# Performance work log

Hardware: AMD Instinct MI355X
Metric: run time of the kernel (lower is better)

The kernel has to match this reference:

```python
import jax, jax.numpy as jnp
import numpy as np

N = 50000
E = 800000
D = 128


def setup_inputs() -> dict:
    key = jax.random.key(0)
    ks = jax.random.split(key, 10)
    x = jax.random.normal(ks[0], (N, D), dtype=jnp.float32)
    edge_index = jax.random.randint(ks[1], (2, E), 0, N, dtype=jnp.int32)
    s = 1.0 / np.sqrt(D)
    W1 = jax.random.uniform(ks[2], (D, D), jnp.float32, -s, s)
    b1 = jnp.zeros((D,), jnp.float32)
    W2 = jax.random.uniform(ks[3], (D, D), jnp.float32, -s, s)
    b2 = jnp.zeros((D,), jnp.float32)
    Wt = jax.random.uniform(ks[4], (D, 1), jnp.float32, -s, s)
    bt = jnp.zeros((1,), jnp.float32)
    We = jax.random.uniform(ks[5], (D, 1), jnp.float32, -s, s)
    be = jnp.zeros((1,), jnp.float32)
    return {"x": x, "edge_index": edge_index, "W1": W1, "b1": b1,
            "W2": W2, "b2": b2, "Wt": Wt, "bt": bt, "We": We, "be": be}


def _gcn_norm(edge_index, n):
    # add self-loops, then symmetric normalization D^-1/2 (A+I) D^-1/2
    loop = jnp.arange(n, dtype=edge_index.dtype)
    src = jnp.concatenate([edge_index[0], loop])
    dst = jnp.concatenate([edge_index[1], loop])
    ones = jnp.ones(src.shape[0], dtype=jnp.float32)
    deg = jax.ops.segment_sum(ones, dst, num_segments=n)
    dinv = jnp.where(deg > 0, jax.lax.rsqrt(deg), 0.0)
    norm = dinv[src] * dinv[dst]  # [E+N]
    return src, dst, norm


def _gcn_conv(h, W, b, src, dst, norm, n):
    h = h @ W                                   # [N, D'] dense GEMM
    msg = h[src] * norm[:, None]                # gather + scale
    out = jax.ops.segment_sum(msg, dst, num_segments=n)  # scatter-add
    return out + b


def reference(x, edge_index, W1, b1, W2, b2, Wt, bt, We, be):
    n = x.shape[0]
    src, dst, norm = _gcn_norm(edge_index, n)
    h = jax.nn.relu(_gcn_conv(x, W1, b1, src, dst, norm, n))
    h = jax.nn.relu(_gcn_conv(h, W2, b2, src, dst, norm, n))
    # dropout is identity at inference (eval mode)
    survival_time = h @ Wt + bt   # [N, 1]
    event_status = h @ We + be    # [N, 1]
    return survival_time, event_status
```

## Files before the change

### kernel.cpp

```cpp
#include <hip/hip_runtime.h>
#include <hip/hip_fp16.h>
#include <math.h>

#define NN 50000
#define NE 800000
#define DD 128

#define NB  196
#define CAP 5300
#define EPB 4096
#define A_BLOCKS 196

#define SLAB2 (NN * 64)

typedef _Float16 half8_t __attribute__((ext_vector_type(8)));
typedef float f32x4 __attribute__((ext_vector_type(4)));


__global__ __launch_bounds__(256) void k_setup(const int* __restrict__ src, const int* __restrict__ dst,
                                               int* __restrict__ bcnt, unsigned int* __restrict__ ebuf,
                                               const float* __restrict__ W1, const float* __restrict__ W2,
                                               __half* __restrict__ WT1, __half* __restrict__ WT2) {
    const int blk = blockIdx.x;
    const int tid = threadIdx.x;

    if (blk < A_BLOCKS) {
        __shared__ int hist[256];
        __shared__ int scanbuf[256];
        __shared__ int gbase[256];
        __shared__ unsigned int stage[EPB];
        __shared__ int tgt[EPB];

        const int e0 = blk * EPB;
        int nE = NE - e0; if (nE > EPB) nE = EPB;

        hist[tid] = 0;
        __syncthreads();

        unsigned int pk[16];
        unsigned int br[16];
        #pragma unroll
        for (int j = 0; j < 16; ++j) {
            int idx = tid + j * 256;
            if (idx < nE) {
                int e = e0 + idx;
                int s = src[e], d = dst[e];
                int b = d >> 8;
                int r = atomicAdd(&hist[b], 1);
                pk[j] = (unsigned int)s | ((unsigned int)(d & 255) << 16);
                br[j] = (unsigned int)b | ((unsigned int)r << 8);
            }
        }
        __syncthreads();
        int v = hist[tid];
        scanbuf[tid] = v;
        __syncthreads();
        for (int o = 1; o < 256; o <<= 1) {
            int t2 = (tid >= o) ? scanbuf[tid - o] : 0;
            __syncthreads();
            scanbuf[tid] += t2;
            __syncthreads();
        }
        int base_excl = scanbuf[tid] - v;
        if (tid < NB && v > 0) gbase[tid] = tid * CAP + atomicAdd(&bcnt[tid], v);
        hist[tid] = base_excl;
        __syncthreads();

        #pragma unroll
        for (int j = 0; j < 16; ++j) {
            int idx = tid + j * 256;
            if (idx < nE) {
                int b = br[j] & 255;
                int r = (int)(br[j] >> 8);
                int pos = hist[b] + r;
                stage[pos] = pk[j];
                tgt[pos]   = gbase[b] + r;
            }
        }
        __syncthreads();
        #pragma unroll
        for (int j = 0; j < 16; ++j) {
            int idx = tid + j * 256;
            if (idx < nE) ebuf[tgt[idx]] = stage[idx];
        }
    } else {
        const float* W  = (blk == A_BLOCKS) ? W1 : W2;
        __half*      WT = (blk == A_BLOCKS) ? WT1 : WT2;
        int n = tid >> 1;
        int k0 = (tid & 1) * 64;
        #pragma unroll 8
        for (int j = 0; j < 64; ++j) {
            int k = k0 + j;
            WT[n * DD + k] = __float2half(W[k * DD + n]);
        }
    }
}


__global__ __launch_bounds__(512) void k_build_csr(const unsigned int* __restrict__ ebuf,
                                                   const int* __restrict__ bcnt,
                                                   int* __restrict__ row_ptr,
                                                   float* __restrict__ dinv,
                                                   unsigned short* __restrict__ col) {
    __shared__ int cnt[256];
    __shared__ int scanb[256];
    __shared__ unsigned short stage[CAP];

    const int b   = blockIdx.x;
    const int tid = threadIdx.x;
    const int seg0 = b * CAP;
    const int sb   = bcnt[b];
    const int n0   = b << 8;
    int nb = NN - n0; if (nb > 256) nb = 256;

    if (tid < 256) scanb[tid] = (tid < NB) ? bcnt[tid] : 0;
    __syncthreads();
    for (int o = 1; o < 256; o <<= 1) {
        int t = 0;
        if (tid < 256 && tid >= o) t = scanb[tid - o];
        __syncthreads();
        if (tid < 256) scanb[tid] += t;
        __syncthreads();
    }
    const int rbase = scanb[b] - sb;
    __syncthreads();

    if (tid < 256) cnt[tid] = 0;
    __syncthreads();
    for (int p = tid; p < sb; p += 512) {
        unsigned int e = ebuf[seg0 + p];
        atomicAdd(&cnt[(e >> 16) & 255], 1);
    }
    __syncthreads();
    int v = (tid < 256) ? cnt[tid] : 0;
    if (tid < 256) scanb[tid] = v;
    __syncthreads();
    for (int o = 1; o < 256; o <<= 1) {
        int t = 0;
        if (tid < 256 && tid >= o) t = scanb[tid - o];
        __syncthreads();
        if (tid < 256) scanb[tid] += t;
        __syncthreads();
    }
    int excl = (tid < 256) ? (scanb[tid] - v) : 0;
    if (tid < nb) {
        row_ptr[n0 + tid] = rbase + excl;
        dinv[n0 + tid] = rsqrtf(1.0f + (float)v);
    }
    if (b == 0 && tid == 0) row_ptr[NN] = NE;
    if (tid < 256) cnt[tid] = excl;
    __syncthreads();
    for (int p = tid; p < sb; p += 512) {
        unsigned int e = ebuf[seg0 + p];
        int pos = atomicAdd(&cnt[(e >> 16) & 255], 1);
        stage[pos] = (unsigned short)(e & 0xFFFFu);
    }
    __syncthreads();
    for (int p = tid; p < sb; p += 512) {
        col[rbase + p] = stage[p];
    }
}


#define LPAD 136
#define GEMM_B 782
#define ZERO_B 98

__global__ __launch_bounds__(256) void k_gemm_x(const float* __restrict__ X, const __half* __restrict__ WT,
                                                const float* __restrict__ dinv, __half* __restrict__ Gc,
                                                float* __restrict__ zbuf, int zcount) {
    const int tid = threadIdx.x;

    if (blockIdx.x >= GEMM_B) {
        int idx = (blockIdx.x - GEMM_B) * 256 + tid;
        if (idx * 4 + 3 < zcount) ((float4*)zbuf)[idx] = make_float4(0.f, 0.f, 0.f, 0.f);
        else {
            for (int k = idx * 4; k < zcount; ++k) zbuf[k] = 0.f;
        }
        return;
    }

    __shared__ __half Wl[DD * LPAD];
    __shared__ __half Al[64 * LPAD];

    const int row0 = blockIdx.x * 64;

    {
        const uint4* WTg = (const uint4*)WT;
        #pragma unroll
        for (int j = 0; j < 8; ++j) {
            int u = tid + j * 256;
            int n = u >> 4, koff = (u & 15) * 8;
            uint4 v = WTg[u];
            *(uint4*)&Wl[n * LPAD + koff] = v;
        }
    }
    {
        const float4* X4 = (const float4*)X;
        #pragma unroll
        for (int j = 0; j < 8; ++j) {
            int u = tid + j * 256;
            int r = u >> 5, c4 = u & 31;
            int grow = row0 + r;
            float4 v = make_float4(0.f, 0.f, 0.f, 0.f);
            if (grow < NN) v = X4[(size_t)grow * 32 + c4];
            __half2 a = __floats2half2_rn(v.x, v.y);
            __half2 b = __floats2half2_rn(v.z, v.w);
            uint2 pk;
            pk.x = *(unsigned int*)&a;
            pk.y = *(unsigned int*)&b;
            *(uint2*)&Al[r * LPAD + c4 * 4] = pk;
        }
    }
    __syncthreads();

    const int wave = tid >> 6;
    const int lane = tid & 63;
    const int m    = lane & 15;
    const int quad = lane >> 4;

    f32x4 acc[8];
    #pragma unroll
    for (int t = 0; t < 8; ++t) acc[t] = (f32x4){0.f, 0.f, 0.f, 0.f};

    #pragma unroll
    for (int kk = 0; kk < DD; kk += 32) {
        half8_t a = *(const half8_t*)&Al[(wave * 16 + m) * LPAD + kk + quad * 8];
        #pragma unroll
        for (int t = 0; t < 8; ++t) {
            half8_t b = *(const half8_t*)&Wl[(t * 16 + m) * LPAD + kk + quad * 8];
            acc[t] = __builtin_amdgcn_mfma_f32_16x16x32_f16(a, b, acc[t], 0, 0, 0);
        }
    }

    __syncthreads();

    float4 dv = *(const float4*)&dinv[row0 + wave * 16 + quad * 4];

    #pragma unroll
    for (int t = 0; t < 8; ++t) {
        #pragma unroll
        for (int r = 0; r < 4; ++r) {
            int row_l = wave * 16 + quad * 4 + r;
            int c     = t * 16 + m;
            float val = acc[t][r] * ((const float*)&dv)[r];
            Al[row_l * LPAD + c] = __float2half(val);
        }
    }
    __syncthreads();

    {
        #pragma unroll
        for (int j = 0; j < 4; ++j) {
            int u = tid + j * 256;
            int r = u >> 4, c16 = u & 15;
            int ch = c16 >> 3, wi = c16 & 7;
            int grow = row0 + r;
            if (grow < NN) {
                uint4 v = *(const uint4*)&Al[r * LPAD + c16 * 8];
                *(uint4*)(Gc + (size_t)ch * SLAB2 + (size_t)grow * 64 + wi * 8) = v;
            }
        }
    }
}


__global__ __launch_bounds__(256) void k_gemm_h(const __half* __restrict__ Xc, const __half* __restrict__ WT,
                                                const float* __restrict__ dinv, __half* __restrict__ Gc) {
    __shared__ __half Wl[DD * LPAD];
    __shared__ __half Al[64 * LPAD];

    const int tid  = threadIdx.x;
    const int row0 = blockIdx.x * 64;

    {
        const uint4* WTg = (const uint4*)WT;
        #pragma unroll
        for (int j = 0; j < 8; ++j) {
            int u = tid + j * 256;
            int n = u >> 4, koff = (u & 15) * 8;
            uint4 v = WTg[u];
            *(uint4*)&Wl[n * LPAD + koff] = v;
        }
    }
    {
        #pragma unroll
        for (int j = 0; j < 4; ++j) {
            int u = tid + j * 256;
            int r = u >> 4, c16 = u & 15;
            int ch = c16 >> 3, wi = c16 & 7;
            int grow = row0 + r;
            uint4 v;
            if (grow < NN) v = *(const uint4*)(Xc + (size_t)ch * SLAB2 + (size_t)grow * 64 + wi * 8);
            else { v.x = 0; v.y = 0; v.z = 0; v.w = 0; }
            *(uint4*)&Al[r * LPAD + c16 * 8] = v;
        }
    }
    __syncthreads();

    const int wave = tid >> 6;
    const int lane = tid & 63;
    const int m    = lane & 15;
    const int quad = lane >> 4;

    f32x4 acc[8];
    #pragma unroll
    for (int t = 0; t < 8; ++t) acc[t] = (f32x4){0.f, 0.f, 0.f, 0.f};

    #pragma unroll
    for (int kk = 0; kk < DD; kk += 32) {
        half8_t a = *(const half8_t*)&Al[(wave * 16 + m) * LPAD + kk + quad * 8];
        #pragma unroll
        for (int t = 0; t < 8; ++t) {
            half8_t b = *(const half8_t*)&Wl[(t * 16 + m) * LPAD + kk + quad * 8];
            acc[t] = __builtin_amdgcn_mfma_f32_16x16x32_f16(a, b, acc[t], 0, 0, 0);
        }
    }

    __syncthreads();

    float4 dv = *(const float4*)&dinv[row0 + wave * 16 + quad * 4];

    #pragma unroll
    for (int t = 0; t < 8; ++t) {
        #pragma unroll
        for (int r = 0; r < 4; ++r) {
            int row_l = wave * 16 + quad * 4 + r;
            int c     = t * 16 + m;
            float val = acc[t][r] * ((const float*)&dv)[r];
            Al[row_l * LPAD + c] = __float2half(val);
        }
    }
    __syncthreads();

    {
        #pragma unroll
        for (int j = 0; j < 4; ++j) {
            int u = tid + j * 256;
            int r = u >> 4, c16 = u & 15;
            int ch = c16 >> 3, wi = c16 & 7;
            int grow = row0 + r;
            if (grow < NN) {
                uint4 v = *(const uint4*)&Al[r * LPAD + c16 * 8];
                *(uint4*)(Gc + (size_t)ch * SLAB2 + (size_t)grow * 64 + wi * 8) = v;
            }
        }
    }
}


__device__ inline float4 h4_to_f4(uint2 r) {
    __half2 a = *(__half2*)&r.x;
    __half2 b = *(__half2*)&r.y;
    float2 lo = __half22float2(a), hi = __half22float2(b);
    return make_float4(lo.x, lo.y, hi.x, hi.y);
}

__device__ inline uint2 f4_to_h4(float4 v) {
    __half2 a = __floats2half2_rn(v.x, v.y);
    __half2 b = __floats2half2_rn(v.z, v.w);
    uint2 r;
    r.x = *(unsigned int*)&a;
    r.y = *(unsigned int*)&b;
    return r;
}

__device__ inline float4 gather_grp64(const __half* __restrict__ slab, int node, int fl,
                                      const unsigned short* __restrict__ col, int beg, int end) {
    const __half* base = slab + fl * 4;
    float4 accA = h4_to_f4(*(const uint2*)(base + (size_t)node * 64));
    float4 accB = make_float4(0.f, 0.f, 0.f, 0.f);
    int p = beg;
    for (; p + 7 < end; p += 8) {
        int s0 = col[p],     s1 = col[p + 1], s2 = col[p + 2], s3 = col[p + 3];
        int s4 = col[p + 4], s5 = col[p + 5], s6 = col[p + 6], s7 = col[p + 7];
        float4 v0 = h4_to_f4(*(const uint2*)(base + (size_t)s0 * 64));
        float4 v1 = h4_to_f4(*(const uint2*)(base + (size_t)s1 * 64));
        float4 v2 = h4_to_f4(*(const uint2*)(base + (size_t)s2 * 64));
        float4 v3 = h4_to_f4(*(const uint2*)(base + (size_t)s3 * 64));
        float4 v4 = h4_to_f4(*(const uint2*)(base + (size_t)s4 * 64));
        float4 v5 = h4_to_f4(*(const uint2*)(base + (size_t)s5 * 64));
        float4 v6 = h4_to_f4(*(const uint2*)(base + (size_t)s6 * 64));
        float4 v7 = h4_to_f4(*(const uint2*)(base + (size_t)s7 * 64));
        accA.x += (v0.x + v1.x) + (v4.x + v5.x);
        accA.y += (v0.y + v1.y) + (v4.y + v5.y);
        accA.z += (v0.z + v1.z) + (v4.z + v5.z);
        accA.w += (v0.w + v1.w) + (v4.w + v5.w);
        accB.x += (v2.x + v3.x) + (v6.x + v7.x);
        accB.y += (v2.y + v3.y) + (v6.y + v7.y);
        accB.z += (v2.z + v3.z) + (v6.z + v7.z);
        accB.w += (v2.w + v3.w) + (v6.w + v7.w);
    }
    if (p + 3 < end) {
        int s0 = col[p], s1 = col[p + 1], s2 = col[p + 2], s3 = col[p + 3];
        float4 v0 = h4_to_f4(*(const uint2*)(base + (size_t)s0 * 64));
        float4 v1 = h4_to_f4(*(const uint2*)(base + (size_t)s1 * 64));
        float4 v2 = h4_to_f4(*(const uint2*)(base + (size_t)s2 * 64));
        float4 v3 = h4_to_f4(*(const uint2*)(base + (size_t)s3 * 64));
        accA.x += v0.x + v1.x; accA.y += v0.y + v1.y; accA.z += v0.z + v1.z; accA.w += v0.w + v1.w;
        accB.x += v2.x + v3.x; accB.y += v2.y + v3.y; accB.z += v2.z + v3.z; accB.w += v2.w + v3.w;
        p += 4;
    }
    for (; p < end; ++p) {
        int s0 = col[p];
        float4 v0 = h4_to_f4(*(const uint2*)(base + (size_t)s0 * 64));
        accA.x += v0.x; accA.y += v0.y; accA.z += v0.z; accA.w += v0.w;
    }
    accA.x += accB.x; accA.y += accB.y; accA.z += accB.z; accA.w += accB.w;
    return accA;
}

__global__ __launch_bounds__(256) void k_aggregate_c(const __half* __restrict__ G, const float* __restrict__ dinv,
                                                     const int* __restrict__ row_ptr, const unsigned short* __restrict__ col,
                                                     const float* __restrict__ bias, __half* __restrict__ H) {
    const int bx    = blockIdx.x;
    const int slot  = bx & 7;
    const int chunk = slot >> 2;
    const int nb    = (bx >> 3) * 4 + (slot & 3);
    const int g     = threadIdx.x >> 4;
    const int fl    = threadIdx.x & 15;
    const int node  = nb * 16 + g;
    if (node >= NN) return;

    const __half* slab = G + (size_t)chunk * SLAB2;
    int beg = row_ptr[node];
    int end = row_ptr[node + 1];
    float4 acc = gather_grp64(slab, node, fl, col, beg, end);

    float di = dinv[node];
    float4 bv = *(const float4*)(bias + chunk * 64 + fl * 4);
    float4 hv;
    hv.x = fmaxf(fmaf(di, acc.x, bv.x), 0.f);
    hv.y = fmaxf(fmaf(di, acc.y, bv.y), 0.f);
    hv.z = fmaxf(fmaf(di, acc.z, bv.z), 0.f);
    hv.w = fmaxf(fmaf(di, acc.w, bv.w), 0.f);
    *(uint2*)(H + (size_t)chunk * SLAB2 + (size_t)node * 64 + fl * 4) = f4_to_h4(hv);
}

__global__ __launch_bounds__(256) void k_aggregate_heads_c(const __half* __restrict__ G, const float* __restrict__ dinv,
                                                           const int* __restrict__ row_ptr, const unsigned short* __restrict__ col,
                                                           const float* __restrict__ bias,
                                                           const float* __restrict__ Wt, const float* __restrict__ bt,
                                                           const float* __restrict__ We, const float* __restrict__ be,
                                                           float* __restrict__ out) {
    const int bx    = blockIdx.x;
    const int slot  = bx & 7;
    const int chunk = slot >> 2;
    const int nb    = (bx >> 3) * 4 + (slot & 3);
    const int g     = threadIdx.x >> 4;
    const int fl    = threadIdx.x & 15;
    const int node  = nb * 16 + g;
    if (node >= NN) return;

    const __half* slab = G + (size_t)chunk * SLAB2;
    int beg = row_ptr[node];
    int end = row_ptr[node + 1];
    float4 acc = gather_grp64(slab, node, fl, col, beg, end);

    float di = dinv[node];
    float4 bv = *(const float4*)(bias + chunk * 64 + fl * 4);
    float hx = fmaxf(fmaf(di, acc.x, bv.x), 0.f);
    float hy = fmaxf(fmaf(di, acc.y, bv.y), 0.f);
    float hz = fmaxf(fmaf(di, acc.z, bv.z), 0.f);
    float hw = fmaxf(fmaf(di, acc.w, bv.w), 0.f);

    float4 wt = *(const float4*)(Wt + chunk * 64 + fl * 4);
    float4 we = *(const float4*)(We + chunk * 64 + fl * 4);
    float t  = hx * wt.x + hy * wt.y + hz * wt.z + hw * wt.w;
    float ev = hx * we.x + hy * we.y + hz * we.z + hw * we.w;
    #pragma unroll
    for (int o = 1; o < 16; o <<= 1) {
        t  += __shfl_xor(t, o, 64);
        ev += __shfl_xor(ev, o, 64);
    }
    if (fl == 0) {
        if (chunk == 0) { t += bt[0]; ev += be[0]; }
        atomicAdd(&out[node], t);
        atomicAdd(&out[NN + node], ev);
    }
}


extern "C" void kernel_launch(void* const* d_in, const int* in_sizes, int n_in,
                              void* d_out, int out_size, void* d_ws, size_t ws_size,
                              hipStream_t stream) {
    const float* x  = (const float*)d_in[0];
    const int*   ei = (const int*)d_in[1];
    const float* W1 = (const float*)d_in[2];
    const float* b1 = (const float*)d_in[3];
    const float* W2 = (const float*)d_in[4];
    const float* b2 = (const float*)d_in[5];
    const float* Wt = (const float*)d_in[6];
    const float* bt = (const float*)d_in[7];
    const float* We = (const float*)d_in[8];
    const float* be = (const float*)d_in[9];
    float* out = (float*)d_out;

    const int* srcI = ei;
    const int* dstI = ei + NE;

    char* w = (char*)d_ws;
    __half*         Gh    = (__half*)w;         w += (size_t)NN * DD * sizeof(__half);
    __half*         H1h   = (__half*)w;         w += (size_t)NN * DD * sizeof(__half);
    __half*         WT1   = (__half*)w;         w += (size_t)DD * DD * sizeof(__half);
    __half*         WT2   = (__half*)w;         w += (size_t)DD * DD * sizeof(__half);
    unsigned int*   ebuf  = (unsigned int*)w;   w += (size_t)NB * CAP * sizeof(unsigned int);
    unsigned short* col   = (unsigned short*)w; w += (size_t)NE * sizeof(unsigned short);
    float*          dinv  = (float*)w;          w += (size_t)(NN + 64) * sizeof(float);
    int*            rowp  = (int*)w;            w += (size_t)(NN + 1) * sizeof(int);
    int*            bcnt  = (int*)w;            w += (size_t)NB * sizeof(int);

    const int SETUP_B = A_BLOCKS + 2;
    const int NBLK    = (NN + 15) / 16;
    const int AGG_B   = ((NBLK + 3) / 4) * 8;

    hipMemsetAsync(bcnt, 0, (size_t)NB * sizeof(int), stream);

    hipLaunchKernelGGL(k_setup,     dim3(SETUP_B), dim3(256), 0, stream,
                       srcI, dstI, bcnt, ebuf, W1, W2, WT1, WT2);
    hipLaunchKernelGGL(k_build_csr, dim3(NB),      dim3(512), 0, stream, ebuf, bcnt, rowp, dinv, col);

    hipLaunchKernelGGL(k_gemm_x,      dim3(GEMM_B + ZERO_B), dim3(256), 0, stream, x, WT1, dinv, Gh, out, out_size);
    hipLaunchKernelGGL(k_aggregate_c, dim3(AGG_B),           dim3(256), 0, stream, Gh, dinv, rowp, col, b1, H1h);

    hipLaunchKernelGGL(k_gemm_h,            dim3(GEMM_B), dim3(256), 0, stream, H1h, WT2, dinv, Gh);
    hipLaunchKernelGGL(k_aggregate_heads_c, dim3(AGG_B),  dim3(256), 0, stream, Gh, dinv, rowp, col, b2,
                       Wt, bt, We, be, out);
}
```

Measured before the change: 202.5 us.

## Pad CSR rows to multiples of eight with dummy node for vectorized gathers

Each CSR row is padded to a multiple of eight neighbors. Padding entries point to a dummy node NN, whose GEMM output row (padded slab NNP) is written unconditionally. This lets the aggregate loop load eight column indices as one uint4 and removes the tail loops and the global row-offset scan. The cost is extra gathers of padding rows and larger col storage, and correctness depends on the dummy row holding zeros, which the GEMM must write from padded input rows.

```diff
diff --git a/kernel.cpp b/kernel.cpp
--- a/kernel.cpp
+++ b/kernel.cpp
@@ -3,15 +3,17 @@
 #include <math.h>
 
 #define NN 50000
+#define NNP 50048
 #define NE 800000
 #define DD 128
 
 #define NB  196
 #define CAP 5300
+#define CAPP 6400
 #define EPB 4096
 #define A_BLOCKS 196
 
-#define SLAB2 (NN * 64)
+#define SLAB2 (NNP * 64)
 
 typedef _Float16 half8_t __attribute__((ext_vector_type(8)));
 typedef float f32x4 __attribute__((ext_vector_type(4)));
@@ -99,12 +101,12 @@
 
 __global__ __launch_bounds__(512) void k_build_csr(const unsigned int* __restrict__ ebuf,
                                                    const int* __restrict__ bcnt,
-                                                   int* __restrict__ row_ptr,
+                                                   int* __restrict__ rowbeg, int* __restrict__ rowend,
                                                    float* __restrict__ dinv,
                                                    unsigned short* __restrict__ col) {
     __shared__ int cnt[256];
     __shared__ int scanb[256];
-    __shared__ unsigned short stage[CAP];
+    __shared__ unsigned short stage[CAPP];
 
     const int b   = blockIdx.x;
     const int tid = threadIdx.x;
@@ -113,7 +115,16 @@
     const int n0   = b << 8;
     int nb = NN - n0; if (nb > 256) nb = 256;
 
-    if (tid < 256) scanb[tid] = (tid < NB) ? bcnt[tid] : 0;
+    if (tid < 256) cnt[tid] = 0;
+    __syncthreads();
+    for (int p = tid; p < sb; p += 512) {
+        unsigned int e = ebuf[seg0 + p];
+        atomicAdd(&cnt[(e >> 16) & 255], 1);
+    }
+    __syncthreads();
+    int v  = (tid < 256) ? cnt[tid] : 0;
+    int pv = (v + 7) & ~7;
+    if (tid < 256) scanb[tid] = pv;
     __syncthreads();
     for (int o = 1; o < 256; o <<= 1) {
         int t = 0;
@@ -122,33 +133,13 @@
         if (tid < 256) scanb[tid] += t;
         __syncthreads();
     }
-    const int rbase = scanb[b] - sb;
-    __syncthreads();
-
-    if (tid < 256) cnt[tid] = 0;
-    __syncthreads();
-    for (int p = tid; p < sb; p += 512) {
-        unsigned int e = ebuf[seg0 + p];
-        atomicAdd(&cnt[(e >> 16) & 255], 1);
-    }
-    __syncthreads();
-    int v = (tid < 256) ? cnt[tid] : 0;
-    if (tid < 256) scanb[tid] = v;
-    __syncthreads();
-    for (int o = 1; o < 256; o <<= 1) {
-        int t = 0;
-        if (tid < 256 && tid >= o) t = scanb[tid - o];
-        __syncthreads();
-        if (tid < 256) scanb[tid] += t;
-        __syncthreads();
-    }
-    int excl = (tid < 256) ? (scanb[tid] - v) : 0;
+    int exclp = (tid < 256) ? (scanb[tid] - pv) : 0;
     if (tid < nb) {
-        row_ptr[n0 + tid] = rbase + excl;
+        rowbeg[n0 + tid] = b * CAPP + exclp;
+        rowend[n0 + tid] = b * CAPP + exclp + pv;
         dinv[n0 + tid] = rsqrtf(1.0f + (float)v);
     }
-    if (b == 0 && tid == 0) row_ptr[NN] = NE;
-    if (tid < 256) cnt[tid] = excl;
+    if (tid < 256) cnt[tid] = exclp;
     __syncthreads();
     for (int p = tid; p < sb; p += 512) {
         unsigned int e = ebuf[seg0 + p];
@@ -156,8 +147,13 @@
         stage[pos] = (unsigned short)(e & 0xFFFFu);
     }
     __syncthreads();
-    for (int p = tid; p < sb; p += 512) {
-        col[rbase + p] = stage[p];
+    if (tid < nb) {
+        for (int k = exclp + v; k < exclp + pv; ++k) stage[k] = (unsigned short)NN;
+    }
+    __syncthreads();
+    const int sbp = scanb[255];
+    for (int p = tid; p < sbp; p += 512) {
+        col[b * CAPP + p] = stage[p];
     }
 }
 
@@ -256,10 +252,8 @@
             int r = u >> 4, c16 = u & 15;
             int ch = c16 >> 3, wi = c16 & 7;
             int grow = row0 + r;
-            if (grow < NN) {
-                uint4 v = *(const uint4*)&Al[r * LPAD + c16 * 8];
-                *(uint4*)(Gc + (size_t)ch * SLAB2 + (size_t)grow * 64 + wi * 8) = v;
-            }
+            uint4 v = *(const uint4*)&Al[r * LPAD + c16 * 8];
+            *(uint4*)(Gc + (size_t)ch * SLAB2 + (size_t)grow * 64 + wi * 8) = v;
         }
     }
 }
@@ -340,10 +334,8 @@
             int r = u >> 4, c16 = u & 15;
             int ch = c16 >> 3, wi = c16 & 7;
             int grow = row0 + r;
-            if (grow < NN) {
-                uint4 v = *(const uint4*)&Al[r * LPAD + c16 * 8];
-                *(uint4*)(Gc + (size_t)ch * SLAB2 + (size_t)grow * 64 + wi * 8) = v;
-            }
+            uint4 v = *(const uint4*)&Al[r * LPAD + c16 * 8];
+            *(uint4*)(Gc + (size_t)ch * SLAB2 + (size_t)grow * 64 + wi * 8) = v;
         }
     }
 }
@@ -370,10 +362,12 @@
     const __half* base = slab + fl * 4;
     float4 accA = h4_to_f4(*(const uint2*)(base + (size_t)node * 64));
     float4 accB = make_float4(0.f, 0.f, 0.f, 0.f);
-    int p = beg;
-    for (; p + 7 < end; p += 8) {
-        int s0 = col[p],     s1 = col[p + 1], s2 = col[p + 2], s3 = col[p + 3];
-        int s4 = col[p + 4], s5 = col[p + 5], s6 = col[p + 6], s7 = col[p + 7];
+    for (int p = beg; p < end; p += 8) {
+        uint4 c8 = *(const uint4*)(col + p);
+        int s0 = c8.x & 0xFFFF, s1 = c8.x >> 16;
+        int s2 = c8.y & 0xFFFF, s3 = c8.y >> 16;
+        int s4 = c8.z & 0xFFFF, s5 = c8.z >> 16;
+        int s6 = c8.w & 0xFFFF, s7 = c8.w >> 16;
         float4 v0 = h4_to_f4(*(const uint2*)(base + (size_t)s0 * 64));
         float4 v1 = h4_to_f4(*(const uint2*)(base + (size_t)s1 * 64));
         float4 v2 = h4_to_f4(*(const uint2*)(base + (size_t)s2 * 64));
@@ -391,27 +385,13 @@
         accB.z += (v2.z + v3.z) + (v6.z + v7.z);
         accB.w += (v2.w + v3.w) + (v6.w + v7.w);
     }
-    if (p + 3 < end) {
-        int s0 = col[p], s1 = col[p + 1], s2 = col[p + 2], s3 = col[p + 3];
-        float4 v0 = h4_to_f4(*(const uint2*)(base + (size_t)s0 * 64));
-        float4 v1 = h4_to_f4(*(const uint2*)(base + (size_t)s1 * 64));
-        float4 v2 = h4_to_f4(*(const uint2*)(base + (size_t)s2 * 64));
-        float4 v3 = h4_to_f4(*(const uint2*)(base + (size_t)s3 * 64));
-        accA.x += v0.x + v1.x; accA.y += v0.y + v1.y; accA.z += v0.z + v1.z; accA.w += v0.w + v1.w;
-        accB.x += v2.x + v3.x; accB.y += v2.y + v3.y; accB.z += v2.z + v3.z; accB.w += v2.w + v3.w;
-        p += 4;
-    }
-    for (; p < end; ++p) {
-        int s0 = col[p];
-        float4 v0 = h4_to_f4(*(const uint2*)(base + (size_t)s0 * 64));
-        accA.x += v0.x; accA.y += v0.y; accA.z += v0.z; accA.w += v0.w;
-    }
     accA.x += accB.x; accA.y += accB.y; accA.z += accB.z; accA.w += accB.w;
     return accA;
 }
 
 __global__ __launch_bounds__(256) void k_aggregate_c(const __half* __restrict__ G, const float* __restrict__ dinv,
-                                                     const int* __restrict__ row_ptr, const unsigned short* __restrict__ col,
+                                                     const int* __restrict__ rowbeg, const int* __restrict__ rowend,
+                                                     const unsigned short* __restrict__ col,
                                                      const float* __restrict__ bias, __half* __restrict__ H) {
     const int bx    = blockIdx.x;
     const int slot  = bx & 7;
@@ -423,8 +403,8 @@
     if (node >= NN) return;
 
     const __half* slab = G + (size_t)chunk * SLAB2;
-    int beg = row_ptr[node];
-    int end = row_ptr[node + 1];
+    int beg = rowbeg[node];
+    int end = rowend[node];
     float4 acc = gather_grp64(slab, node, fl, col, beg, end);
 
     float di = dinv[node];
@@ -438,7 +418,8 @@
 }
 
 __global__ __launch_bounds__(256) void k_aggregate_heads_c(const __half* __restrict__ G, const float* __restrict__ dinv,
-                                                           const int* __restrict__ row_ptr, const unsigned short* __restrict__ col,
+                                                           const int* __restrict__ rowbeg, const int* __restrict__ rowend,
+                                                           const unsigned short* __restrict__ col,
                                                            const float* __restrict__ bias,
                                                            const float* __restrict__ Wt, const float* __restrict__ bt,
                                                            const float* __restrict__ We, const float* __restrict__ be,
@@ -453,8 +434,8 @@
     if (node >= NN) return;
 
     const __half* slab = G + (size_t)chunk * SLAB2;
-    int beg = row_ptr[node];
-    int end = row_ptr[node + 1];
+    int beg = rowbeg[node];
+    int end = rowend[node];
     float4 acc = gather_grp64(slab, node, fl, col, beg, end);
 
     float di = dinv[node];
@@ -500,14 +481,15 @@
     const int* dstI = ei + NE;
 
     char* w = (char*)d_ws;
-    __half*         Gh    = (__half*)w;         w += (size_t)NN * DD * sizeof(__half);
-    __half*         H1h   = (__half*)w;         w += (size_t)NN * DD * sizeof(__half);
+    __half*         Gh    = (__half*)w;         w += (size_t)2 * SLAB2 * sizeof(__half);
+    __half*         H1h   = (__half*)w;         w += (size_t)2 * SLAB2 * sizeof(__half);
     __half*         WT1   = (__half*)w;         w += (size_t)DD * DD * sizeof(__half);
     __half*         WT2   = (__half*)w;         w += (size_t)DD * DD * sizeof(__half);
     unsigned int*   ebuf  = (unsigned int*)w;   w += (size_t)NB * CAP * sizeof(unsigned int);
-    unsigned short* col   = (unsigned short*)w; w += (size_t)NE * sizeof(unsigned short);
+    unsigned short* col   = (unsigned short*)w; w += (size_t)NB * CAPP * sizeof(unsigned short);
     float*          dinv  = (float*)w;          w += (size_t)(NN + 64) * sizeof(float);
-    int*            rowp  = (int*)w;            w += (size_t)(NN + 1) * sizeof(int);
+    int*            rowbeg= (int*)w;            w += (size_t)NN * sizeof(int);
+    int*            rowend= (int*)w;            w += (size_t)NN * sizeof(int);
     int*            bcnt  = (int*)w;            w += (size_t)NB * sizeof(int);
 
     const int SETUP_B = A_BLOCKS + 2;
@@ -518,12 +500,12 @@
 
     hipLaunchKernelGGL(k_setup,     dim3(SETUP_B), dim3(256), 0, stream,
                        srcI, dstI, bcnt, ebuf, W1, W2, WT1, WT2);
-    hipLaunchKernelGGL(k_build_csr, dim3(NB),      dim3(512), 0, stream, ebuf, bcnt, rowp, dinv, col);
+    hipLaunchKernelGGL(k_build_csr, dim3(NB),      dim3(512), 0, stream, ebuf, bcnt, rowbeg, rowend, dinv, col);
 
     hipLaunchKernelGGL(k_gemm_x,      dim3(GEMM_B + ZERO_B), dim3(256), 0, stream, x, WT1, dinv, Gh, out, out_size);
-    hipLaunchKernelGGL(k_aggregate_c, dim3(AGG_B),           dim3(256), 0, stream, Gh, dinv, rowp, col, b1, H1h);
+    hipLaunchKernelGGL(k_aggregate_c, dim3(AGG_B),           dim3(256), 0, stream, Gh, dinv, rowbeg, rowend, col, b1, H1h);
 
     hipLaunchKernelGGL(k_gemm_h,            dim3(GEMM_B), dim3(256), 0, stream, H1h, WT2, dinv, Gh);
-    hipLaunchKernelGGL(k_aggregate_heads_c, dim3(AGG_B),  dim3(256), 0, stream, Gh, dinv, rowp, col, b2,
+    hipLaunchKernelGGL(k_aggregate_heads_c, dim3(AGG_B),  dim3(256), 0, stream, Gh, dinv, rowbeg, rowend, col, b2,
                        Wt, bt, We, be, out);
 }
```

New measurement: 183.8 us. -9.2%, faster.
